# Optimization experiments

Measured on AMD Instinct MI355X. Metric: run time of the kernel, lower is better.

The kernel has to match this reference:

```python
import jax, jax.numpy as jnp
import numpy as np


def gcn_conv(x, src, dst, ew, W, b):
    """PyG GCNConv with edge weights: add self-loops, symmetric deg norm,
    x @ W then normalized scatter-add aggregation, plus bias."""
    N = x.shape[0]
    loop = jnp.arange(N)
    src2 = jnp.concatenate([src, loop])
    dst2 = jnp.concatenate([dst, loop])
    ew2 = jnp.concatenate([ew, jnp.ones((N,), dtype=x.dtype)])
    deg = jax.ops.segment_sum(ew2, dst2, num_segments=N)
    dis = jnp.where(deg > 0, jax.lax.rsqrt(jnp.maximum(deg, 1e-30)), 0.0)
    norm = dis[src2] * ew2 * dis[dst2]            # [E+N]
    h = x @ W                                      # [N, F]
    msg = h[src2] * norm[:, None]                  # gather + scale
    out = jax.ops.segment_sum(msg, dst2, num_segments=N)  # scatter-add
    return out + b


def setup_inputs() -> dict:
    key = jax.random.key(0)
    ks = jax.random.split(key, 12)
    N, F, E, H = 50000, 128, 625000, 121
    x = jax.random.normal(ks[0], (N, F), dtype=jnp.float32)
    edge_index = jax.random.randint(ks[1], (2, E), 0, N, dtype=jnp.int64)
    edge_attr = jax.random.uniform(ks[2], (E,), dtype=jnp.float32)
    s = 1.0 / np.sqrt(F)
    W1 = jax.random.uniform(ks[3], (F, F), minval=-s, maxval=s)
    b1 = jnp.zeros((F,), dtype=jnp.float32)
    W2 = jax.random.uniform(ks[4], (F, F), minval=-s, maxval=s)
    b2 = jnp.zeros((F,), dtype=jnp.float32)
    lw1 = jax.random.uniform(ks[5], (F, H), minval=-s, maxval=s)
    lb1 = jax.random.uniform(ks[6], (H,), minval=-s, maxval=s)
    sh = 1.0 / np.sqrt(H)
    lw2 = jax.random.uniform(ks[7], (H, 1), minval=-sh, maxval=sh)
    lb2 = jax.random.uniform(ks[8], (1,), minval=-sh, maxval=sh)
    return {"x": x, "edge_index": edge_index, "edge_attr": edge_attr,
            "W1": W1, "b1": b1, "W2": W2, "b2": b2,
            "lw1": lw1, "lb1": lb1, "lw2": lw2, "lb2": lb2}


def reference(x, edge_index, edge_attr, W1, b1, W2, b2, lw1, lb1, lw2, lb2):
    src, dst = edge_index[0], edge_index[1]
    h = jax.nn.relu(gcn_conv(x, src, dst, edge_attr, W1, b1))
    h = jax.nn.relu(gcn_conv(h, src, dst, edge_attr, W2, b2))
    g = jnp.mean(h, axis=0)                        # graph readout [F]
    g = jax.nn.relu(g @ lw1 + lb1)
    return g @ lw2 + lb2                           # [1]
```

## Files before the change

### kernel.cpp

```cpp
#include <hip/hip_runtime.h>
#include <hip/hip_bf16.h>

#define FDIM 128
#define ELLW 64
#define CHUNK 4096
#define BKTSH 8
#define CAP 4096

typedef unsigned int uint;
typedef unsigned short ushort;
typedef unsigned char uchar;
typedef __attribute__((ext_vector_type(8))) short bf16x8;
typedef __attribute__((ext_vector_type(4))) float f32x4;

__device__ __forceinline__ ushort f2bf(float f) {
    uint u = __float_as_uint(f);
    return (ushort)((u + 0x7fffu + ((u >> 16) & 1u)) >> 16);
}
__device__ __forceinline__ float bfhi(uint v) { return __uint_as_float(v & 0xffff0000u); }
__device__ __forceinline__ uchar f2fp8(float f) {
    return (uchar)(__builtin_amdgcn_cvt_pk_fp8_f32(f, 0.f, 0, false) & 0xff);
}

__global__ void prep(const float* __restrict__ W1, const float* __restrict__ W2,
                     ushort* __restrict__ wt1, ushort* __restrict__ wt2,
                     int* __restrict__ gcursor, int nbkt) {
    int i = blockIdx.x * 256 + threadIdx.x;
    if (i < 16384) {
        int k = i >> 7, c = i & 127;
        wt1[c * FDIM + k] = f2bf(W1[i]);
    } else {
        int j = i - 16384;
        int k = j >> 7, c = j & 127;
        wt2[c * FDIM + k] = f2bf(W2[j]);
    }
    if (i < nbkt) gcursor[i] = i * CAP;
}

__global__ __launch_bounds__(256)
void build_p1(const int* __restrict__ srcs, const int* __restrict__ dsts,
              const float* __restrict__ ew, int* gcursor,
              uint2* __restrict__ part, int E, int nbkt) {
    __shared__ int hist[256];
    __shared__ int gbase[256];
    __shared__ int cur[256];
    int tid = threadIdx.x;
    hist[tid] = 0;
    __syncthreads();
    int base = blockIdx.x * CHUNK;
    #pragma unroll
    for (int i = 0; i < CHUNK / 256; ++i) {
        int e = base + i * 256 + tid;
        if (e < E) atomicAdd(&hist[dsts[e] >> BKTSH], 1);
    }
    __syncthreads();
    if (tid < nbkt && hist[tid] > 0)
        gbase[tid] = atomicAdd(&gcursor[tid], hist[tid]);
    cur[tid] = 0;
    __syncthreads();
    #pragma unroll
    for (int i = 0; i < CHUNK / 256; ++i) {
        int e = base + i * 256 + tid;
        if (e < E) {
            int d = dsts[e];
            int bkt = d >> BKTSH;
            int pos = atomicAdd(&cur[bkt], 1);
            long gp = (long)gbase[bkt] + pos;
            if (gp < (long)(bkt + 1) * CAP)
                part[gp] = make_uint2(((uint)f2bf(ew[e]) << 16) | (uint)srcs[e],
                                      (uint)d);
        }
    }
}

__global__ __launch_bounds__(256)
void build_p2(const uint2* __restrict__ part, const int* __restrict__ gcursor,
              uint* __restrict__ ell, int* __restrict__ cnt,
              float* __restrict__ dis, int N) {
    __shared__ int lcur[256];
    __shared__ float ldeg[256];
    int tid = threadIdx.x;
    int b = blockIdx.x;
    lcur[tid] = 0; ldeg[tid] = 0.f;
    __syncthreads();
    int start = b * CAP;
    int end = min(gcursor[b], start + CAP);
    for (int e = start + tid; e < end; e += 256) {
        uint2 pe = part[e];
        int li = (int)pe.y - (b << BKTSH);
        int r = atomicAdd(&lcur[li], 1);
        if (r < ELLW) ell[(long)pe.y * ELLW + r] = pe.x;
        atomicAdd(&ldeg[li], bfhi(pe.x));
    }
    __syncthreads();
    int d = (b << BKTSH) + tid;
    if (d < N) {
        cnt[d] = min(lcur[tid], ELLW);
        dis[d] = rsqrtf(1.0f + ldeg[tid]);
    }
}

template<int IN_BF16>
__global__ __launch_bounds__(256) void gemm_mfma(const void* __restrict__ Ap,
                                                 const ushort* __restrict__ Wt,
                                                 const float* __restrict__ dis,
                                                 uchar* __restrict__ Hb, int N) {
    int lane = threadIdx.x & 63;
    int wave = threadIdx.x >> 6;
    int row0 = blockIdx.x * 64 + wave * 16;
    int m = lane & 15;
    int ko = (lane >> 4) << 3;
    int row = row0 + m;

    f32x4 acc[8];
    #pragma unroll
    for (int n = 0; n < 8; ++n) acc[n] = (f32x4){0.f, 0.f, 0.f, 0.f};

    #pragma unroll 1
    for (int kc = 0; kc < FDIM; kc += 32) {
        bf16x8 a = (bf16x8)(short)0;
        if (row < N) {
            if (IN_BF16) {
                a = *(const bf16x8*)((const ushort*)Ap + (long)row * FDIM + kc + ko);
            } else {
                const float* A = (const float*)Ap;
                float4 f0 = *(const float4*)(A + (long)row * FDIM + kc + ko);
                float4 f1 = *(const float4*)(A + (long)row * FDIM + kc + ko + 4);
                a[0] = (short)f2bf(f0.x); a[1] = (short)f2bf(f0.y);
                a[2] = (short)f2bf(f0.z); a[3] = (short)f2bf(f0.w);
                a[4] = (short)f2bf(f1.x); a[5] = (short)f2bf(f1.y);
                a[6] = (short)f2bf(f1.z); a[7] = (short)f2bf(f1.w);
            }
        }
        #pragma unroll
        for (int n = 0; n < 8; ++n) {
            bf16x8 b = *(const bf16x8*)(Wt + (n * 16 + m) * FDIM + kc + ko);
            acc[n] = __builtin_amdgcn_mfma_f32_16x16x32_bf16(a, b, acc[n], 0, 0, 0);
        }
    }

    int rbase = (lane >> 4) << 2;
    #pragma unroll
    for (int r = 0; r < 4; ++r) {
        int gr = row0 + rbase + r;
        if (gr < N) {
            float sc = dis[gr];
            #pragma unroll
            for (int n = 0; n < 8; ++n)
                Hb[(long)gr * FDIM + n * 16 + m] = f2fp8(acc[n][r] * sc);
        }
    }
}

__device__ __forceinline__ void cvt4_acc(uint4 u, float wv,
                                         float4& a0, float4& a1,
                                         float4& a2, float4& a3) {
    auto lo0 = __builtin_amdgcn_cvt_pk_f32_fp8(u.x, false);
    auto hi0 = __builtin_amdgcn_cvt_pk_f32_fp8(u.x, true);
    auto lo1 = __builtin_amdgcn_cvt_pk_f32_fp8(u.y, false);
    auto hi1 = __builtin_amdgcn_cvt_pk_f32_fp8(u.y, true);
    auto lo2 = __builtin_amdgcn_cvt_pk_f32_fp8(u.z, false);
    auto hi2 = __builtin_amdgcn_cvt_pk_f32_fp8(u.z, true);
    auto lo3 = __builtin_amdgcn_cvt_pk_f32_fp8(u.w, false);
    auto hi3 = __builtin_amdgcn_cvt_pk_f32_fp8(u.w, true);
    a0.x = fmaf(lo0[0], wv, a0.x); a0.y = fmaf(lo0[1], wv, a0.y);
    a0.z = fmaf(hi0[0], wv, a0.z); a0.w = fmaf(hi0[1], wv, a0.w);
    a1.x = fmaf(lo1[0], wv, a1.x); a1.y = fmaf(lo1[1], wv, a1.y);
    a1.z = fmaf(hi1[0], wv, a1.z); a1.w = fmaf(hi1[1], wv, a1.w);
    a2.x = fmaf(lo2[0], wv, a2.x); a2.y = fmaf(lo2[1], wv, a2.y);
    a2.z = fmaf(hi2[0], wv, a2.z); a2.w = fmaf(hi2[1], wv, a2.w);
    a3.x = fmaf(lo3[0], wv, a3.x); a3.y = fmaf(lo3[1], wv, a3.y);
    a3.z = fmaf(hi3[0], wv, a3.z); a3.w = fmaf(hi3[1], wv, a3.w);
}

template<int FUSE>
__global__ __launch_bounds__(256)
void aggregate(const uchar* __restrict__ hb,
               const float* __restrict__ dis,
               const float* __restrict__ b,
               const int* __restrict__ cnt,
               const uint* __restrict__ ell,
               ushort* __restrict__ Ob,
               float* __restrict__ partial, int N) {
    __shared__ float red[32][FDIM];
    int tid = threadIdx.x;
    int lane = tid & 7;
    int grp = tid >> 3;
    int d = blockIdx.x * 32 + grp;
    int c0 = lane * 16;
    float4 o0, o1, o2, o3;

    if (d < N) {
        float dd = dis[d];
        float4 bv0 = ((const float4*)b)[lane * 4];
        float4 bv1 = ((const float4*)b)[lane * 4 + 1];
        float4 bv2 = ((const float4*)b)[lane * 4 + 2];
        float4 bv3 = ((const float4*)b)[lane * 4 + 3];
        const uint4* row4 = (const uint4*)(ell + (long)d * ELLW);
        int end = min(cnt[d], ELLW);
        float4 a0 = make_float4(0.f, 0.f, 0.f, 0.f);
        float4 a1 = a0, a2 = a0, a3 = a0;
        int k = 0;
        for (; k + 3 < end; k += 4) {
            uint4 ev = row4[k >> 2];
            int s0 = ev.x & 0xffff, s1 = ev.y & 0xffff;
            int s2 = ev.z & 0xffff, s3 = ev.w & 0xffff;
            float w0 = bfhi(ev.x), w1 = bfhi(ev.y);
            float w2 = bfhi(ev.z), w3 = bfhi(ev.w);
            uint4 u0 = *(const uint4*)(hb + (long)s0 * FDIM + c0);
            uint4 u1 = *(const uint4*)(hb + (long)s1 * FDIM + c0);
            uint4 u2 = *(const uint4*)(hb + (long)s2 * FDIM + c0);
            uint4 u3 = *(const uint4*)(hb + (long)s3 * FDIM + c0);
            cvt4_acc(u0, w0, a0, a1, a2, a3);
            cvt4_acc(u1, w1, a0, a1, a2, a3);
            cvt4_acc(u2, w2, a0, a1, a2, a3);
            cvt4_acc(u3, w3, a0, a1, a2, a3);
        }
        const uint* row = ell + (long)d * ELLW;
        for (; k < end; ++k) {
            uint e0 = row[k];
            int s0 = e0 & 0xffff;
            float w0 = bfhi(e0);
            uint4 u0 = *(const uint4*)(hb + (long)s0 * FDIM + c0);
            cvt4_acc(u0, w0, a0, a1, a2, a3);
        }
        uint4 ud = *(const uint4*)(hb + (long)d * FDIM + c0);
        cvt4_acc(ud, 1.0f, a0, a1, a2, a3);
        o0.x = fmaxf(fmaf(a0.x, dd, bv0.x), 0.f);
        o0.y = fmaxf(fmaf(a0.y, dd, bv0.y), 0.f);
        o0.z = fmaxf(fmaf(a0.z, dd, bv0.z), 0.f);
        o0.w = fmaxf(fmaf(a0.w, dd, bv0.w), 0.f);
        o1.x = fmaxf(fmaf(a1.x, dd, bv1.x), 0.f);
        o1.y = fmaxf(fmaf(a1.y, dd, bv1.y), 0.f);
        o1.z = fmaxf(fmaf(a1.z, dd, bv1.z), 0.f);
        o1.w = fmaxf(fmaf(a1.w, dd, bv1.w), 0.f);
        o2.x = fmaxf(fmaf(a2.x, dd, bv2.x), 0.f);
        o2.y = fmaxf(fmaf(a2.y, dd, bv2.y), 0.f);
        o2.z = fmaxf(fmaf(a2.z, dd, bv2.z), 0.f);
        o2.w = fmaxf(fmaf(a2.w, dd, bv2.w), 0.f);
        o3.x = fmaxf(fmaf(a3.x, dd, bv3.x), 0.f);
        o3.y = fmaxf(fmaf(a3.y, dd, bv3.y), 0.f);
        o3.z = fmaxf(fmaf(a3.z, dd, bv3.z), 0.f);
        o3.w = fmaxf(fmaf(a3.w, dd, bv3.w), 0.f);
        if (!FUSE) {
            uint4 ov;
            ov.x = (uint)f2bf(o0.x) | ((uint)f2bf(o0.y) << 16);
            ov.y = (uint)f2bf(o0.z) | ((uint)f2bf(o0.w) << 16);
            ov.z = (uint)f2bf(o1.x) | ((uint)f2bf(o1.y) << 16);
            ov.w = (uint)f2bf(o1.z) | ((uint)f2bf(o1.w) << 16);
            *(uint4*)(Ob + (long)d * FDIM + c0) = ov;
            ov.x = (uint)f2bf(o2.x) | ((uint)f2bf(o2.y) << 16);
            ov.y = (uint)f2bf(o2.z) | ((uint)f2bf(o2.w) << 16);
            ov.z = (uint)f2bf(o3.x) | ((uint)f2bf(o3.y) << 16);
            ov.w = (uint)f2bf(o3.z) | ((uint)f2bf(o3.w) << 16);
            *(uint4*)(Ob + (long)d * FDIM + c0 + 8) = ov;
        }
    } else {
        o0 = make_float4(0.f, 0.f, 0.f, 0.f);
        o1 = o0; o2 = o0; o3 = o0;
    }

    if (FUSE) {
        *(float4*)&red[grp][c0]      = o0;
        *(float4*)&red[grp][c0 + 4]  = o1;
        *(float4*)&red[grp][c0 + 8]  = o2;
        *(float4*)&red[grp][c0 + 12] = o3;
        __syncthreads();
        if (tid < FDIM) {
            float s = 0.f;
            #pragma unroll
            for (int g = 0; g < 32; ++g) s += red[g][tid];
            partial[(long)blockIdx.x * FDIM + tid] = s;
        }
    }
}

__global__ void reduce_g(const float* __restrict__ partial,
                         float* __restrict__ partial2, int nb) {
    __shared__ float sd[2][FDIM];
    int col = threadIdx.x & 127;
    int half = threadIdx.x >> 7;
    float s = 0.f;
    for (int r = blockIdx.x * 2 + half; r < nb; r += 128)
        s += partial[(long)r * FDIM + col];
    sd[half][col] = s;
    __syncthreads();
    if (threadIdx.x < FDIM)
        partial2[(long)blockIdx.x * FDIM + col] = sd[0][col] + sd[1][col];
}

__global__ void mlp_head(const float* __restrict__ partial2,
                         const float* __restrict__ lw1,
                         const float* __restrict__ lb1,
                         const float* __restrict__ lw2,
                         const float* __restrict__ lb2,
                         float* __restrict__ out, float invN, int H) {
    __shared__ float gs[FDIM];
    __shared__ float red[FDIM];
    int t = threadIdx.x;
    float s = 0.f;
    #pragma unroll 8
    for (int r = 0; r < 64; ++r) s += partial2[r * FDIM + t];
    gs[t] = s * invN;
    __syncthreads();
    float p = 0.f;
    if (t < H) {
        float acc = lb1[t];
        #pragma unroll 8
        for (int f = 0; f < FDIM; ++f)
            acc = fmaf(gs[f], lw1[f * H + t], acc);
        p = fmaxf(acc, 0.f) * lw2[t];
    }
    red[t] = p;
    __syncthreads();
    for (int st = 64; st > 0; st >>= 1) {
        if (t < st) red[t] += red[t + st];
        __syncthreads();
    }
    if (t == 0) out[0] = red[0] + lb2[0];
}

extern "C" void kernel_launch(void* const* d_in, const int* in_sizes, int n_in,
                              void* d_out, int out_size, void* d_ws, size_t ws_size,
                              hipStream_t stream) {
    const float* x   = (const float*)d_in[0];
    const int*   eix = (const int*)d_in[1];
    const float* ea  = (const float*)d_in[2];
    const float* W1  = (const float*)d_in[3];
    const float* b1  = (const float*)d_in[4];
    const float* W2  = (const float*)d_in[5];
    const float* b2  = (const float*)d_in[6];
    const float* lw1 = (const float*)d_in[7];
    const float* lb1 = (const float*)d_in[8];
    const float* lw2 = (const float*)d_in[9];
    const float* lb2 = (const float*)d_in[10];

    const int N = in_sizes[0] / FDIM;
    const int E = in_sizes[2];
    const int H = in_sizes[8];
    const int* srcs = eix;
    const int* dsts = eix + E;

    int nAgg = (N + 31) / 32;
    int nbkt = (N + 255) >> 8;

    uchar*  hb      = (uchar*)d_ws;
    ushort* ob      = (ushort*)(hb + (long)N * FDIM);
    ushort* wt1     = ob + (long)N * FDIM;
    ushort* wt2     = wt1 + FDIM * FDIM;
    float*  partial = (float*)(wt2 + FDIM * FDIM);
    float*  partial2= partial + (long)nAgg * FDIM;
    float*  dis     = partial2 + 64 * FDIM;
    uint*   ell     = (uint*)(dis + N);
    int*    cnt     = (int*)(ell + (long)N * ELLW);
    int*    gcursor = cnt + N;
    uint2*  part    = (uint2*)(gcursor + ((nbkt + 1) & ~1));

    float* outv = (float*)d_out;

    int gemmBlocks = (N + 63) / 64;
    int p1Blocks = (E + CHUNK - 1) / CHUNK;

    prep<<<128, 256, 0, stream>>>(W1, W2, wt1, wt2, gcursor, nbkt);
    build_p1<<<p1Blocks, 256, 0, stream>>>(srcs, dsts, ea, gcursor, part, E, nbkt);
    build_p2<<<nbkt, 256, 0, stream>>>(part, gcursor, ell, cnt, dis, N);

    gemm_mfma<0><<<gemmBlocks, 256, 0, stream>>>(x, wt1, dis, hb, N);
    aggregate<0><<<nAgg, 256, 0, stream>>>(hb, dis, b1, cnt, ell, ob, partial, N);

    gemm_mfma<1><<<gemmBlocks, 256, 0, stream>>>(ob, wt2, dis, hb, N);
    aggregate<1><<<nAgg, 256, 0, stream>>>(hb, dis, b2, cnt, ell, ob, partial, N);

    reduce_g<<<64, 256, 0, stream>>>(partial, partial2, nAgg);
    mlp_head<<<1, FDIM, 0, stream>>>(partial2, lw1, lb1, lw2, lb2, outv,
                                     1.0f / (float)N, H);
}
```

Baseline: 134.4 us.

## Pad ELL rows to multiples of 8 and fuse global readout via atomics

Build pads each ELL row with zero-weight entries up to a multiple of 8 so aggregation can run an 8-wide unrolled gather loop with no scalar tail. The per-block partial readout buffer and separate reduce kernel are replaced by atomicAdd into a zeroed 128-float accumulator consumed directly by the MLP head. This removes one kernel launch and a tail loop but adds padded gathers to row 0 and atomic contention on 128 addresses.

```diff
diff --git a/kernel.cpp b/kernel.cpp
--- a/kernel.cpp
+++ b/kernel.cpp
@@ -24,7 +24,7 @@
 
 __global__ void prep(const float* __restrict__ W1, const float* __restrict__ W2,
                      ushort* __restrict__ wt1, ushort* __restrict__ wt2,
-                     int* __restrict__ gcursor, int nbkt) {
+                     int* __restrict__ gcursor, float* __restrict__ g, int nbkt) {
     int i = blockIdx.x * 256 + threadIdx.x;
     if (i < 16384) {
         int k = i >> 7, c = i & 127;
@@ -35,6 +35,7 @@
         wt2[c * FDIM + k] = f2bf(W2[j]);
     }
     if (i < nbkt) gcursor[i] = i * CAP;
+    if (i < FDIM) g[i] = 0.f;
 }
 
 __global__ __launch_bounds__(256)
@@ -95,7 +96,10 @@
     __syncthreads();
     int d = (b << BKTSH) + tid;
     if (d < N) {
-        cnt[d] = min(lcur[tid], ELLW);
+        int c = min(lcur[tid], ELLW);
+        int cp = (c + 7) & ~7;
+        for (int r = c; r < cp; ++r) ell[(long)d * ELLW + r] = 0;
+        cnt[d] = cp;
         dis[d] = rsqrtf(1.0f + ldeg[tid]);
     }
 }
@@ -181,7 +185,7 @@
                const int* __restrict__ cnt,
                const uint* __restrict__ ell,
                ushort* __restrict__ Ob,
-               float* __restrict__ partial, int N) {
+               float* __restrict__ g, int N) {
     __shared__ float red[32][FDIM];
     int tid = threadIdx.x;
     int lane = tid & 7;
@@ -197,32 +201,32 @@
         float4 bv2 = ((const float4*)b)[lane * 4 + 2];
         float4 bv3 = ((const float4*)b)[lane * 4 + 3];
         const uint4* row4 = (const uint4*)(ell + (long)d * ELLW);
-        int end = min(cnt[d], ELLW);
+        int end = cnt[d];
         float4 a0 = make_float4(0.f, 0.f, 0.f, 0.f);
         float4 a1 = a0, a2 = a0, a3 = a0;
-        int k = 0;
-        for (; k + 3 < end; k += 4) {
-            uint4 ev = row4[k >> 2];
-            int s0 = ev.x & 0xffff, s1 = ev.y & 0xffff;
-            int s2 = ev.z & 0xffff, s3 = ev.w & 0xffff;
-            float w0 = bfhi(ev.x), w1 = bfhi(ev.y);
-            float w2 = bfhi(ev.z), w3 = bfhi(ev.w);
+        for (int k = 0; k < end; k += 8) {
+            uint4 ev0 = row4[k >> 2];
+            uint4 ev1 = row4[(k >> 2) + 1];
+            int s0 = ev0.x & 0xffff, s1 = ev0.y & 0xffff;
+            int s2 = ev0.z & 0xffff, s3 = ev0.w & 0xffff;
+            int s4 = ev1.x & 0xffff, s5 = ev1.y & 0xffff;
+            int s6 = ev1.z & 0xffff, s7 = ev1.w & 0xffff;
             uint4 u0 = *(const uint4*)(hb + (long)s0 * FDIM + c0);
             uint4 u1 = *(const uint4*)(hb + (long)s1 * FDIM + c0);
             uint4 u2 = *(const uint4*)(hb + (long)s2 * FDIM + c0);
             uint4 u3 = *(const uint4*)(hb + (long)s3 * FDIM + c0);
-            cvt4_acc(u0, w0, a0, a1, a2, a3);
-            cvt4_acc(u1, w1, a0, a1, a2, a3);
-            cvt4_acc(u2, w2, a0, a1, a2, a3);
-            cvt4_acc(u3, w3, a0, a1, a2, a3);
-        }
-        const uint* row = ell + (long)d * ELLW;
-        for (; k < end; ++k) {
-            uint e0 = row[k];
-            int s0 = e0 & 0xffff;
-            float w0 = bfhi(e0);
-            uint4 u0 = *(const uint4*)(hb + (long)s0 * FDIM + c0);
-            cvt4_acc(u0, w0, a0, a1, a2, a3);
+            uint4 u4 = *(const uint4*)(hb + (long)s4 * FDIM + c0);
+            uint4 u5 = *(const uint4*)(hb + (long)s5 * FDIM + c0);
+            uint4 u6 = *(const uint4*)(hb + (long)s6 * FDIM + c0);
+            uint4 u7 = *(const uint4*)(hb + (long)s7 * FDIM + c0);
+            cvt4_acc(u0, bfhi(ev0.x), a0, a1, a2, a3);
+            cvt4_acc(u1, bfhi(ev0.y), a0, a1, a2, a3);
+            cvt4_acc(u2, bfhi(ev0.z), a0, a1, a2, a3);
+            cvt4_acc(u3, bfhi(ev0.w), a0, a1, a2, a3);
+            cvt4_acc(u4, bfhi(ev1.x), a0, a1, a2, a3);
+            cvt4_acc(u5, bfhi(ev1.y), a0, a1, a2, a3);
+            cvt4_acc(u6, bfhi(ev1.z), a0, a1, a2, a3);
+            cvt4_acc(u7, bfhi(ev1.w), a0, a1, a2, a3);
         }
         uint4 ud = *(const uint4*)(hb + (long)d * FDIM + c0);
         cvt4_acc(ud, 1.0f, a0, a1, a2, a3);
@@ -269,27 +273,13 @@
         if (tid < FDIM) {
             float s = 0.f;
             #pragma unroll
-            for (int g = 0; g < 32; ++g) s += red[g][tid];
-            partial[(long)blockIdx.x * FDIM + tid] = s;
-        }
-    }
-}
-
-__global__ void reduce_g(const float* __restrict__ partial,
-                         float* __restrict__ partial2, int nb) {
-    __shared__ float sd[2][FDIM];
-    int col = threadIdx.x & 127;
-    int half = threadIdx.x >> 7;
-    float s = 0.f;
-    for (int r = blockIdx.x * 2 + half; r < nb; r += 128)
-        s += partial[(long)r * FDIM + col];
-    sd[half][col] = s;
-    __syncthreads();
-    if (threadIdx.x < FDIM)
-        partial2[(long)blockIdx.x * FDIM + col] = sd[0][col] + sd[1][col];
-}
-
-__global__ void mlp_head(const float* __restrict__ partial2,
+            for (int gi = 0; gi < 32; ++gi) s += red[gi][tid];
+            atomicAdd(&g[tid], s);
+        }
+    }
+}
+
+__global__ void mlp_head(const float* __restrict__ g,
                          const float* __restrict__ lw1,
                          const float* __restrict__ lb1,
                          const float* __restrict__ lw2,
@@ -298,10 +288,7 @@
     __shared__ float gs[FDIM];
     __shared__ float red[FDIM];
     int t = threadIdx.x;
-    float s = 0.f;
-    #pragma unroll 8
-    for (int r = 0; r < 64; ++r) s += partial2[r * FDIM + t];
-    gs[t] = s * invN;
+    gs[t] = g[t] * invN;
     __syncthreads();
     float p = 0.f;
     if (t < H) {
@@ -348,10 +335,9 @@
     ushort* ob      = (ushort*)(hb + (long)N * FDIM);
     ushort* wt1     = ob + (long)N * FDIM;
     ushort* wt2     = wt1 + FDIM * FDIM;
-    float*  partial = (float*)(wt2 + FDIM * FDIM);
-    float*  partial2= partial + (long)nAgg * FDIM;
-    float*  dis     = partial2 + 64 * FDIM;
-    uint*   ell     = (uint*)(dis + N);
+    float*  dis     = (float*)(wt2 + FDIM * FDIM);
+    float*  g       = dis + N;
+    uint*   ell     = (uint*)(g + FDIM);
     int*    cnt     = (int*)(ell + (long)N * ELLW);
     int*    gcursor = cnt + N;
     uint2*  part    = (uint2*)(gcursor + ((nbkt + 1) & ~1));
@@ -361,17 +347,16 @@
     int gemmBlocks = (N + 63) / 64;
     int p1Blocks = (E + CHUNK - 1) / CHUNK;
 
-    prep<<<128, 256, 0, stream>>>(W1, W2, wt1, wt2, gcursor, nbkt);
+    prep<<<128, 256, 0, stream>>>(W1, W2, wt1, wt2, gcursor, g, nbkt);
     build_p1<<<p1Blocks, 256, 0, stream>>>(srcs, dsts, ea, gcursor, part, E, nbkt);
     build_p2<<<nbkt, 256, 0, stream>>>(part, gcursor, ell, cnt, dis, N);
 
     gemm_mfma<0><<<gemmBlocks, 256, 0, stream>>>(x, wt1, dis, hb, N);
-    aggregate<0><<<nAgg, 256, 0, stream>>>(hb, dis, b1, cnt, ell, ob, partial, N);
+    aggregate<0><<<nAgg, 256, 0, stream>>>(hb, dis, b1, cnt, ell, ob, g, N);
 
     gemm_mfma<1><<<gemmBlocks, 256, 0, stream>>>(ob, wt2, dis, hb, N);
-    aggregate<1><<<nAgg, 256, 0, stream>>>(hb, dis, b2, cnt, ell, ob, partial, N);
-
-    reduce_g<<<64, 256, 0, stream>>>(partial, partial2, nAgg);
-    mlp_head<<<1, FDIM, 0, stream>>>(partial2, lw1, lb1, lw2, lb2, outv,
+    aggregate<1><<<nAgg, 256, 0, stream>>>(hb, dis, b2, cnt, ell, ob, g, N);
+
+    mlp_head<<<1, FDIM, 0, stream>>>(g, lw1, lb1, lw2, lb2, outv,
                                      1.0f / (float)N, H);
 }
```

Result: slower. 158.0 us (+17.5%).
